# Kernel tuning notes

Measured on AMD Instinct MI355X. Metric: run time of the kernel, lower is better.

Reference implementation:

```python
import jax, jax.numpy as jnp
import numpy as np

DIM = 768
NUM_HEADS = 12

def setup_inputs() -> dict:
    key = jax.random.key(0)
    ks = jax.random.split(key, 8)
    B, N, C = 16, 3136, DIM
    x = jax.random.normal(ks[0], (B, N, C), dtype=jnp.float32)
    # nn.Linear(dim, 3*dim): y = x @ W^T + b; store W already transposed [C, 3C]
    qkv_w = jax.random.normal(ks[1], (C, 3 * C), dtype=jnp.float32) * (C ** -0.5)
    qkv_b = jax.random.normal(ks[2], (3 * C,), dtype=jnp.float32) * 0.02
    # depthwise Conv2d(dim, dim, 3, padding=1, groups=dim): kernel OIHW [C,1,3,3]
    dw_w = jax.random.normal(ks[3], (C, 1, 3, 3), dtype=jnp.float32) * (1.0 / 3.0)
    dw_b = jax.random.normal(ks[4], (C,), dtype=jnp.float32) * 0.02
    proj_w = jax.random.normal(ks[5], (C, C), dtype=jnp.float32) * (C ** -0.5)
    proj_b = jax.random.normal(ks[6], (C,), dtype=jnp.float32) * 0.02
    return {"x": x, "qkv_w": qkv_w, "qkv_b": qkv_b, "dw_w": dw_w,
            "dw_b": dw_b, "proj_w": proj_w, "proj_b": proj_b}

def reference(x, qkv_w, qkv_b, dw_w, dw_b, proj_w, proj_b):
    B, N, C = x.shape
    H = NUM_HEADS
    d = C // H
    scale = d ** -0.5
    qkv = (x @ qkv_w + qkv_b).reshape(B, N, 3, H, d).transpose(2, 0, 3, 1, 4)
    q, k, v = qkv[0], qkv[1], qkv[2]  # each [B,H,N,d]
    q = jax.nn.relu(q) * scale
    k = jax.nn.relu(k)
    # linear attention: context = k^T @ v  -> [B,H,d,d]
    context = jnp.einsum('bhnd,bhne->bhde', k, v)
    out = jnp.einsum('bhnd,bhde->bhne', q, context)  # [B,H,N,d]
    out = out.transpose(0, 2, 1, 3).reshape(B, N, C)
    hw = int(N ** 0.5)  # N is a perfect square token grid
    img = out.transpose(0, 2, 1).reshape(B, C, hw, hw)
    img = jax.lax.conv_general_dilated(
        img, dw_w, window_strides=(1, 1), padding='SAME',
        feature_group_count=C,
        dimension_numbers=('NCHW', 'OIHW', 'NCHW')) + dw_b[None, :, None, None]
    out = img.reshape(B, C, N).transpose(0, 2, 1)
    return out @ proj_w + proj_b
```

## Files before the change

### kernel.cpp

```cpp
#include <hip/hip_runtime.h>

typedef unsigned short ushort_t;
typedef __attribute__((ext_vector_type(8))) short short8;
typedef __attribute__((ext_vector_type(4))) float f32x4;

#define DEV __device__ __forceinline__

DEV unsigned short f2bf(float f) {
  unsigned int u = __float_as_uint(f);
  u += 0x7FFFu + ((u >> 16) & 1u);
  return (unsigned short)(u >> 16);
}
DEV float bf2f(unsigned short h) { return __uint_as_float(((unsigned int)h) << 16); }

DEV void gload_lds16(const void* g, void* l) {
  __builtin_amdgcn_global_load_lds((const __attribute__((address_space(1))) void*)g,
                                   (__attribute__((address_space(3))) void*)l, 16, 0, 0);
}

__global__ void cvt_x_k(const float4* __restrict__ in, ushort4* __restrict__ out) {
  const int i = blockIdx.x * 256 + threadIdx.x;
  float4 f = in[i];
  out[i] = make_ushort4(f2bf(f.x), f2bf(f.y), f2bf(f.z), f2bf(f.w));
}

__global__ __launch_bounds__(256)
void transp_k(const float* __restrict__ in, ushort_t* __restrict__ out, int R, int Cn) {
  __shared__ float tile[32][33];
  const int ctiles = Cn >> 5;
  const int bx = blockIdx.x % ctiles;
  const int by = blockIdx.x / ctiles;
  const int tx = threadIdx.x & 31, ty = threadIdx.x >> 5;
  #pragma unroll
  for (int i = 0; i < 4; ++i) {
    const int r = by * 32 + ty + i * 8;
    tile[ty + i * 8][tx] = in[(size_t)r * Cn + bx * 32 + tx];
  }
  __syncthreads();
  #pragma unroll
  for (int i = 0; i < 4; ++i) {
    const int cc = bx * 32 + ty + i * 8;
    out[(size_t)cc * R + by * 32 + tx] = f2bf(tile[tx][ty + i * 8]);
  }
}

template <int MODE>
__global__ __launch_bounds__(256, 2)
void gemm_bt(const ushort_t* __restrict__ A, const ushort_t* __restrict__ BT,
             const float* __restrict__ bias,
             void* __restrict__ o0, void* __restrict__ o1, void* __restrict__ o2,
             int K, int ntiles) {
  constexpr int BK = 32;
  __shared__ __attribute__((aligned(16))) ushort_t As[128 * BK];
  __shared__ __attribute__((aligned(16))) ushort_t Bs[128 * BK];
  const int bid = blockIdx.x;
  const int nt = bid % ntiles, mt = bid / ntiles;
  const int t = threadIdx.x;
  const int w = t >> 6, l = t & 63;
  const int wr = w >> 1, wc = w & 1;
  const int lr = l & 15, lg = l >> 4;

  const ushort_t* Ap = A + (size_t)mt * 128 * K;
  const ushort_t* Bp = BT + (size_t)nt * 128 * K;

  f32x4 acc[4][4];
  #pragma unroll
  for (int i = 0; i < 4; ++i)
    #pragma unroll
    for (int j = 0; j < 4; ++j) acc[i][j] = (f32x4){0.f, 0.f, 0.f, 0.f};

  const int srow = t >> 2;
  const int scol = (t & 3) * 8;

  for (int k0 = 0; k0 < K; k0 += BK) {
    gload_lds16(Ap + (size_t)srow * K + k0 + scol,        &As[srow * BK + scol]);
    gload_lds16(Ap + (size_t)(srow + 64) * K + k0 + scol, &As[(srow + 64) * BK + scol]);
    gload_lds16(Bp + (size_t)srow * K + k0 + scol,        &Bs[srow * BK + scol]);
    gload_lds16(Bp + (size_t)(srow + 64) * K + k0 + scol, &Bs[(srow + 64) * BK + scol]);
    __syncthreads();
    short8 a[4], bfr[4];
    #pragma unroll
    for (int mf = 0; mf < 4; ++mf)
      a[mf] = *(const short8*)&As[(wr * 64 + mf * 16 + lr) * BK + lg * 8];
    #pragma unroll
    for (int nf = 0; nf < 4; ++nf)
      bfr[nf] = *(const short8*)&Bs[(wc * 64 + nf * 16 + lr) * BK + lg * 8];
    #pragma unroll
    for (int mf = 0; mf < 4; ++mf)
      #pragma unroll
      for (int nf = 0; nf < 4; ++nf)
        acc[mf][nf] = __builtin_amdgcn_mfma_f32_16x16x32_bf16(a[mf], bfr[nf], acc[mf][nf], 0, 0, 0);
    __syncthreads();
  }

  if (MODE == 0) {
    ushort_t* q  = (ushort_t*)o0;
    ushort_t* kT = (ushort_t*)o1;
    ushort_t* vT = (ushort_t*)o2;
    #pragma unroll
    for (int nf = 0; nf < 4; ++nf) {
      const int c3 = nt * 128 + wc * 64 + nf * 16 + lr;
      const float bv = bias[c3];
      const int s = c3 / 768;
      const int rem = c3 - s * 768;
      const int h = rem >> 6, dd = rem & 63;
      #pragma unroll
      for (int mf = 0; mf < 4; ++mf) {
        const int mbase = mt * 128 + wr * 64 + mf * 16 + lg * 4;
        #pragma unroll
        for (int r = 0; r < 4; ++r) {
          const int m = mbase + r;
          const int b_ = m / 3136;
          const int n = m - b_ * 3136;
          float v = acc[mf][nf][r] + bv;
          if (s == 0) {
            v = fmaxf(v, 0.f) * 0.125f;
            q[(((size_t)b_ * 12 + h) * 3136 + n) * 64 + dd] = f2bf(v);
          } else if (s == 1) {
            v = fmaxf(v, 0.f);
            kT[(((size_t)b_ * 12 + h) * 64 + dd) * 3136 + n] = f2bf(v);
          } else {
            vT[(((size_t)b_ * 12 + h) * 64 + dd) * 3136 + n] = f2bf(v);
          }
        }
      }
    }
  } else {
    float* O = (float*)o0;
    #pragma unroll
    for (int nf = 0; nf < 4; ++nf) {
      const int c = nt * 128 + wc * 64 + nf * 16 + lr;
      const float bv = bias[c];
      #pragma unroll
      for (int mf = 0; mf < 4; ++mf) {
        const int mbase = mt * 128 + wr * 64 + mf * 16 + lg * 4;
        #pragma unroll
        for (int r = 0; r < 4; ++r)
          O[(size_t)(mbase + r) * 768 + c] = acc[mf][nf][r] + bv;
      }
    }
  }
}

__global__ __launch_bounds__(64)
void ctx_k(const ushort_t* __restrict__ kT, const ushort_t* __restrict__ vT,
           float* __restrict__ ctxT) {
  __shared__ __attribute__((aligned(16))) ushort_t Ks[64 * 64];
  __shared__ __attribute__((aligned(16))) ushort_t Vs[64 * 64];
  const int bid = blockIdx.x;
  const int s = bid % 7, bh = bid / 7;
  const int n0 = s * 448;
  const int t = threadIdx.x;
  const int lr = t & 15, lg = t >> 4;
  const ushort_t* kp = kT + (size_t)bh * 64 * 3136;
  const ushort_t* vp = vT + (size_t)bh * 64 * 3136;
  const int srow = t >> 3, scol = (t & 7) * 8;

  f32x4 acc[4][4];
  #pragma unroll
  for (int i = 0; i < 4; ++i)
    #pragma unroll
    for (int j = 0; j < 4; ++j) acc[i][j] = (f32x4){0.f, 0.f, 0.f, 0.f};

  for (int c = 0; c < 7; ++c) {
    const int nb = n0 + c * 64;
    #pragma unroll
    for (int i = 0; i < 8; ++i) {
      gload_lds16(kp + (size_t)(i * 8 + srow) * 3136 + nb + scol, &Ks[(i * 8 + srow) * 64 + scol]);
      gload_lds16(vp + (size_t)(i * 8 + srow) * 3136 + nb + scol, &Vs[(i * 8 + srow) * 64 + scol]);
    }
    __syncthreads();
    #pragma unroll
    for (int kk = 0; kk < 2; ++kk) {
      short8 a[4], bfr[4];
      #pragma unroll
      for (int mf = 0; mf < 4; ++mf)
        a[mf] = *(const short8*)&Ks[(mf * 16 + lr) * 64 + kk * 32 + lg * 8];
      #pragma unroll
      for (int nf = 0; nf < 4; ++nf)
        bfr[nf] = *(const short8*)&Vs[(nf * 16 + lr) * 64 + kk * 32 + lg * 8];
      #pragma unroll
      for (int mf = 0; mf < 4; ++mf)
        #pragma unroll
        for (int nf = 0; nf < 4; ++nf)
          acc[mf][nf] = __builtin_amdgcn_mfma_f32_16x16x32_bf16(a[mf], bfr[nf], acc[mf][nf], 0, 0, 0);
    }
    __syncthreads();
  }
  float* cp = ctxT + (size_t)bh * 4096;
  #pragma unroll
  for (int mf = 0; mf < 4; ++mf)
    #pragma unroll
    for (int nf = 0; nf < 4; ++nf)
      #pragma unroll
      for (int r = 0; r < 4; ++r)
        atomicAdd(&cp[(nf * 16 + lr) * 64 + mf * 16 + lg * 4 + r], acc[mf][nf][r]);
}

__global__ __launch_bounds__(256)
void attnout_k(const ushort_t* __restrict__ q, const float* __restrict__ ctxT,
               ushort_t* __restrict__ out) {
  __shared__ __attribute__((aligned(16))) ushort_t Qs[256 * 64];
  __shared__ __attribute__((aligned(16))) ushort_t Cs[64 * 64];
  const int bid = blockIdx.x;
  const int tile = bid % 13, bh = bid / 13;
  const int b_ = bh / 12, h = bh - b_ * 12;
  const int n0 = tile * 256;
  const int t = threadIdx.x;
  const int w = t >> 6, l = t & 63;
  const int lr = l & 15, lg = l >> 4;
  const ushort_t* qp = q + (size_t)bh * 3136 * 64;

  {
    const float4* cp = (const float4*)(ctxT + (size_t)bh * 4096);
    #pragma unroll
    for (int i = 0; i < 4; ++i) {
      const int j = i * 256 + t;
      float4 f = cp[j];
      ((ushort4*)Cs)[j] = make_ushort4(f2bf(f.x), f2bf(f.y), f2bf(f.z), f2bf(f.w));
    }
  }
  const int srow = t >> 3, scol = (t & 7) * 8;
  #pragma unroll
  for (int i = 0; i < 8; ++i)
    gload_lds16(qp + (size_t)(n0 + i * 32 + srow) * 64 + scol, &Qs[(i * 32 + srow) * 64 + scol]);
  __syncthreads();

  f32x4 acc[4][4];
  #pragma unroll
  for (int i = 0; i < 4; ++i)
    #pragma unroll
    for (int j = 0; j < 4; ++j) acc[i][j] = (f32x4){0.f, 0.f, 0.f, 0.f};

  #pragma unroll
  for (int kk = 0; kk < 2; ++kk) {
    short8 a[4], bfr[4];
    #pragma unroll
    for (int mf = 0; mf < 4; ++mf)
      a[mf] = *(const short8*)&Qs[(w * 64 + mf * 16 + lr) * 64 + kk * 32 + lg * 8];
    #pragma unroll
    for (int nf = 0; nf < 4; ++nf)
      bfr[nf] = *(const short8*)&Cs[(nf * 16 + lr) * 64 + kk * 32 + lg * 8];
    #pragma unroll
    for (int mf = 0; mf < 4; ++mf)
      #pragma unroll
      for (int nf = 0; nf < 4; ++nf)
        acc[mf][nf] = __builtin_amdgcn_mfma_f32_16x16x32_bf16(a[mf], bfr[nf], acc[mf][nf], 0, 0, 0);
  }

  ushort_t* op = out + (size_t)b_ * 3136 * 768 + h * 64;
  #pragma unroll
  for (int mf = 0; mf < 4; ++mf) {
    const int nb = n0 + w * 64 + mf * 16 + lg * 4;
    #pragma unroll
    for (int r = 0; r < 4; ++r) {
      const int n = nb + r;
      if (n < 3136) {
        #pragma unroll
        for (int nf = 0; nf < 4; ++nf)
          op[(size_t)n * 768 + nf * 16 + lr] = f2bf(acc[mf][nf][r]);
      }
    }
  }
}

__global__ __launch_bounds__(768)
void dwconv_k(const ushort_t* __restrict__ in, const float* __restrict__ w9,
              const float* __restrict__ wb, ushort_t* __restrict__ out) {
  const int bn = blockIdx.x;
  const int b_ = bn / 3136, n = bn - b_ * 3136;
  const int y = n / 56, x = n - y * 56;
  const int c = threadIdx.x;
  const ushort_t* ip = in + (size_t)b_ * 3136 * 768 + c;
  float wv[9];
  #pragma unroll
  for (int i = 0; i < 9; ++i) wv[i] = w9[c * 9 + i];
  float acc = wb[c];
  #pragma unroll
  for (int dy = 0; dy < 3; ++dy) {
    const int yy = y + dy - 1;
    if ((unsigned)yy < 56u) {
      #pragma unroll
      for (int dx = 0; dx < 3; ++dx) {
        const int xx = x + dx - 1;
        if ((unsigned)xx < 56u)
          acc += bf2f(ip[(size_t)(yy * 56 + xx) * 768]) * wv[dy * 3 + dx];
      }
    }
  }
  out[(size_t)bn * 768 + c] = f2bf(acc);
}

extern "C" void kernel_launch(void* const* d_in, const int* in_sizes, int n_in,
                              void* d_out, int out_size, void* d_ws, size_t ws_size,
                              hipStream_t stream) {
  (void)in_sizes; (void)n_in; (void)out_size; (void)ws_size;
  const float* x      = (const float*)d_in[0];
  const float* qkv_w  = (const float*)d_in[1];
  const float* qkv_b  = (const float*)d_in[2];
  const float* dw_w   = (const float*)d_in[3];
  const float* dw_b   = (const float*)d_in[4];
  const float* proj_w = (const float*)d_in[5];
  const float* proj_b = (const float*)d_in[6];
  float* out = (float*)d_out;

  char* ws = (char*)d_ws;
  const size_t SZ = (size_t)50176 * 768 * 2;
  ushort_t* xbf  = (ushort_t*)(ws);
  ushort_t* attn = xbf;
  ushort_t* q    = (ushort_t*)(ws + SZ);
  ushort_t* cvo  = q;
  ushort_t* kT   = (ushort_t*)(ws + 2 * SZ);
  ushort_t* vT   = (ushort_t*)(ws + 3 * SZ);
  ushort_t* wt1  = (ushort_t*)(ws + 4 * SZ);
  ushort_t* wt2  = (ushort_t*)(ws + 4 * SZ + 3538944);
  float*    ctx  = (float*)(ws + 4 * SZ + 3538944 + 1179648);

  hipMemsetAsync(ctx, 0, (size_t)192 * 4096 * 4, stream);
  cvt_x_k<<<37632, 256, 0, stream>>>((const float4*)x, (ushort4*)xbf);
  transp_k<<<1728, 256, 0, stream>>>(qkv_w, wt1, 768, 2304);
  transp_k<<<576, 256, 0, stream>>>(proj_w, wt2, 768, 768);
  gemm_bt<0><<<392 * 18, 256, 0, stream>>>(xbf, wt1, qkv_b, q, kT, vT, 768, 18);
  ctx_k<<<192 * 7, 64, 0, stream>>>(kT, vT, ctx);
  attnout_k<<<192 * 13, 256, 0, stream>>>(q, ctx, attn);
  dwconv_k<<<50176, 768, 0, stream>>>(attn, dw_w, dw_b, cvo);
  gemm_bt<1><<<392 * 6, 256, 0, stream>>>(cvo, wt2, proj_b, out, nullptr, nullptr, 768, 6);
}
```

Before: 1.100 ms.

## Replace 128x128 GEMM with double-buffered swizzled 256x256 tile kernel

New measurement: 1.133 ms. 3.0% more time.

```diff
diff --git a/kernel.cpp b/kernel.cpp
--- a/kernel.cpp
+++ b/kernel.cpp
@@ -45,51 +45,97 @@
 }
 
 template <int MODE>
-__global__ __launch_bounds__(256, 2)
-void gemm_bt(const ushort_t* __restrict__ A, const ushort_t* __restrict__ BT,
+__global__ __launch_bounds__(512, 2)
+void gemm256(const ushort_t* __restrict__ A, const ushort_t* __restrict__ BT,
              const float* __restrict__ bias,
              void* __restrict__ o0, void* __restrict__ o1, void* __restrict__ o2,
              int K, int ntiles) {
-  constexpr int BK = 32;
-  __shared__ __attribute__((aligned(16))) ushort_t As[128 * BK];
-  __shared__ __attribute__((aligned(16))) ushort_t Bs[128 * BK];
-  const int bid = blockIdx.x;
+  __shared__ __attribute__((aligned(16))) ushort_t As[2][16384];
+  __shared__ __attribute__((aligned(16))) ushort_t Bs[2][16384];
+
+  const int nwg = gridDim.x;
+  const int qq = nwg >> 3, rr = nwg & 7;
+  const int xcd = blockIdx.x & 7;
+  const int idx = blockIdx.x >> 3;
+  const int bid = (xcd < rr ? xcd * (qq + 1) : rr * (qq + 1) + (xcd - rr) * qq) + idx;
   const int nt = bid % ntiles, mt = bid / ntiles;
+
   const int t = threadIdx.x;
   const int w = t >> 6, l = t & 63;
-  const int wr = w >> 1, wc = w & 1;
+  const int wr = w >> 2, wc = w & 3;
   const int lr = l & 15, lg = l >> 4;
 
-  const ushort_t* Ap = A + (size_t)mt * 128 * K;
-  const ushort_t* Bp = BT + (size_t)nt * 128 * K;
-
-  f32x4 acc[4][4];
-  #pragma unroll
-  for (int i = 0; i < 4; ++i)
+  const ushort_t* Ap = A + (size_t)mt * 256 * K;
+  const ushort_t* Bp = BT + (size_t)nt * 256 * K;
+
+  const int srow = t >> 3;
+  const int scb  = (t & 7) * 16;
+  const int gcb = scb ^ ((srow & 7) << 4);
+
+  f32x4 acc[8][4];
+  #pragma unroll
+  for (int i = 0; i < 8; ++i)
     #pragma unroll
     for (int j = 0; j < 4; ++j) acc[i][j] = (f32x4){0.f, 0.f, 0.f, 0.f};
 
-  const int srow = t >> 2;
-  const int scol = (t & 3) * 8;
-
-  for (int k0 = 0; k0 < K; k0 += BK) {
-    gload_lds16(Ap + (size_t)srow * K + k0 + scol,        &As[srow * BK + scol]);
-    gload_lds16(Ap + (size_t)(srow + 64) * K + k0 + scol, &As[(srow + 64) * BK + scol]);
-    gload_lds16(Bp + (size_t)srow * K + k0 + scol,        &Bs[srow * BK + scol]);
-    gload_lds16(Bp + (size_t)(srow + 64) * K + k0 + scol, &Bs[(srow + 64) * BK + scol]);
-    __syncthreads();
-    short8 a[4], bfr[4];
-    #pragma unroll
-    for (int mf = 0; mf < 4; ++mf)
-      a[mf] = *(const short8*)&As[(wr * 64 + mf * 16 + lr) * BK + lg * 8];
-    #pragma unroll
-    for (int nf = 0; nf < 4; ++nf)
-      bfr[nf] = *(const short8*)&Bs[(wc * 64 + nf * 16 + lr) * BK + lg * 8];
-    #pragma unroll
-    for (int mf = 0; mf < 4; ++mf)
-      #pragma unroll
-      for (int nf = 0; nf < 4; ++nf)
-        acc[mf][nf] = __builtin_amdgcn_mfma_f32_16x16x32_bf16(a[mf], bfr[nf], acc[mf][nf], 0, 0, 0);
+  const int NT = K >> 6;
+
+  #pragma unroll
+  for (int j = 0; j < 4; ++j) {
+    const int row = j * 64 + srow;
+    gload_lds16(Ap + (size_t)row * K + (gcb >> 1), &As[0][row * 64 + (scb >> 1)]);
+    gload_lds16(Bp + (size_t)row * K + (gcb >> 1), &Bs[0][row * 64 + (scb >> 1)]);
+  }
+  __syncthreads();
+
+  for (int kt = 0; kt < NT; ++kt) {
+    const int cur = kt & 1;
+    if (kt + 1 < NT) {
+      const int k0 = (kt + 1) << 6;
+      #pragma unroll
+      for (int j = 0; j < 4; ++j) {
+        const int row = j * 64 + srow;
+        gload_lds16(Ap + (size_t)row * K + k0 + (gcb >> 1),
+                    &As[cur ^ 1][row * 64 + (scb >> 1)]);
+        gload_lds16(Bp + (size_t)row * K + k0 + (gcb >> 1),
+                    &Bs[cur ^ 1][row * 64 + (scb >> 1)]);
+      }
+    }
+    short8 bf[4][2];
+    #pragma unroll
+    for (int nf = 0; nf < 4; ++nf) {
+      const int rb = wc * 64 + nf * 16 + lr;
+      const int xr = (rb & 7) << 4;
+      #pragma unroll
+      for (int ks = 0; ks < 2; ++ks) {
+        const int kb = ks * 64 + lg * 16;
+        bf[nf][ks] = *(const short8*)&Bs[cur][rb * 64 + ((kb ^ xr) >> 1)];
+      }
+    }
+    #pragma unroll
+    for (int qm = 0; qm < 2; ++qm) {
+      short8 af[4][2];
+      #pragma unroll
+      for (int mf = 0; mf < 4; ++mf) {
+        const int ra = wr * 128 + qm * 64 + mf * 16 + lr;
+        const int xr = (ra & 7) << 4;
+        #pragma unroll
+        for (int ks = 0; ks < 2; ++ks) {
+          const int kb = ks * 64 + lg * 16;
+          af[mf][ks] = *(const short8*)&As[cur][ra * 64 + ((kb ^ xr) >> 1)];
+        }
+      }
+      __builtin_amdgcn_s_setprio(1);
+      #pragma unroll
+      for (int mf = 0; mf < 4; ++mf)
+        #pragma unroll
+        for (int nf = 0; nf < 4; ++nf)
+          #pragma unroll
+          for (int ks = 0; ks < 2; ++ks)
+            acc[qm * 4 + mf][nf] = __builtin_amdgcn_mfma_f32_16x16x32_bf16(
+                af[mf][ks], bf[nf][ks], acc[qm * 4 + mf][nf], 0, 0, 0);
+      __builtin_amdgcn_s_setprio(0);
+    }
     __syncthreads();
   }
 
@@ -99,20 +145,20 @@
     ushort_t* vT = (ushort_t*)o2;
     #pragma unroll
     for (int nf = 0; nf < 4; ++nf) {
-      const int c3 = nt * 128 + wc * 64 + nf * 16 + lr;
+      const int c3 = nt * 256 + wc * 64 + nf * 16 + lr;
       const float bv = bias[c3];
-      const int s = c3 / 768;
+      const int s = (c3 >= 1536) ? 2 : (c3 >= 768 ? 1 : 0);
       const int rem = c3 - s * 768;
       const int h = rem >> 6, dd = rem & 63;
       #pragma unroll
-      for (int mf = 0; mf < 4; ++mf) {
-        const int mbase = mt * 128 + wr * 64 + mf * 16 + lg * 4;
+      for (int mi = 0; mi < 8; ++mi) {
+        const int mbase = mt * 256 + wr * 128 + mi * 16 + lg * 4;
         #pragma unroll
         for (int r = 0; r < 4; ++r) {
           const int m = mbase + r;
           const int b_ = m / 3136;
           const int n = m - b_ * 3136;
-          float v = acc[mf][nf][r] + bv;
+          float v = acc[mi][nf][r] + bv;
           if (s == 0) {
             v = fmaxf(v, 0.f) * 0.125f;
             q[(((size_t)b_ * 12 + h) * 3136 + n) * 64 + dd] = f2bf(v);
@@ -129,14 +175,14 @@
     float* O = (float*)o0;
     #pragma unroll
     for (int nf = 0; nf < 4; ++nf) {
-      const int c = nt * 128 + wc * 64 + nf * 16 + lr;
+      const int c = nt * 256 + wc * 64 + nf * 16 + lr;
       const float bv = bias[c];
       #pragma unroll
-      for (int mf = 0; mf < 4; ++mf) {
-        const int mbase = mt * 128 + wr * 64 + mf * 16 + lg * 4;
+      for (int mi = 0; mi < 8; ++mi) {
+        const int mbase = mt * 256 + wr * 128 + mi * 16 + lg * 4;
         #pragma unroll
         for (int r = 0; r < 4; ++r)
-          O[(size_t)(mbase + r) * 768 + c] = acc[mf][nf][r] + bv;
+          O[(size_t)(mbase + r) * 768 + c] = acc[mi][nf][r] + bv;
       }
     }
   }
@@ -320,9 +366,9 @@
   cvt_x_k<<<37632, 256, 0, stream>>>((const float4*)x, (ushort4*)xbf);
   transp_k<<<1728, 256, 0, stream>>>(qkv_w, wt1, 768, 2304);
   transp_k<<<576, 256, 0, stream>>>(proj_w, wt2, 768, 768);
-  gemm_bt<0><<<392 * 18, 256, 0, stream>>>(xbf, wt1, qkv_b, q, kT, vT, 768, 18);
+  gemm256<0><<<196 * 9, 512, 0, stream>>>(xbf, wt1, qkv_b, q, kT, vT, 768, 9);
   ctx_k<<<192 * 7, 64, 0, stream>>>(kT, vT, ctx);
   attnout_k<<<192 * 13, 256, 0, stream>>>(q, ctx, attn);
   dwconv_k<<<50176, 768, 0, stream>>>(attn, dw_w, dw_b, cvo);
-  gemm_bt<1><<<392 * 6, 256, 0, stream>>>(cvo, wt2, proj_b, out, nullptr, nullptr, 768, 6);
-}
+  gemm256<1><<<196 * 3, 512, 0, stream>>>(cvo, wt2, proj_b, out, nullptr, nullptr, 768, 3);
+}
```
